# Optimization experiments

Hardware: AMD Instinct MI355X
Metric: run time of the kernel (lower is better)

Reference implementation:

```python
import jax, jax.numpy as jnp
import numpy as np

REG = 0.1          # entropic regularization, as in the module
N_ITERS = 100      # fixed Sinkhorn iteration count (POT numItermax capped; see notes)


def _sqdist(x, y):
    # ot.dist default: squared Euclidean pairwise distances, [n, m]
    x2 = jnp.sum(x * x, axis=1)[:, None]
    y2 = jnp.sum(y * y, axis=1)[None, :]
    M = x2 + y2 - 2.0 * (x @ y.T)
    return jnp.maximum(M, 0.0)


def setup_inputs() -> dict:
    key = jax.random.key(0)
    kx, ky = jax.random.split(key)
    n, m, d = 4096, 4096, 32
    # uniform in [0, 0.5) keeps exp(-M/reg) representable in fp32
    x = jax.random.uniform(kx, (n, d), dtype=jnp.float32) * 0.5
    y = jax.random.uniform(ky, (m, d), dtype=jnp.float32) * 0.5
    return {"x": x, "y": y}


def reference(x, y):
    n, m = x.shape[0], y.shape[0]
    a = jnp.full((n,), 1.0 / n, dtype=x.dtype)   # uniform source marginal
    b = jnp.full((m,), 1.0 / m, dtype=y.dtype)   # uniform target marginal
    M = _sqdist(x, y)                            # [n, m] cost
    K = jnp.exp(-M / REG)                        # [n, m] Gibbs kernel

    u0 = jnp.full((n,), 1.0 / n, dtype=x.dtype)
    v0 = jnp.full((m,), 1.0 / m, dtype=y.dtype)

    def step(carry, _):
        u, v = carry
        u = a / (K @ v)      # [n]
        v = b / (K.T @ u)    # [m]
        return (u, v), None

    (u, v), _ = jax.lax.scan(step, (u0, v0), None, length=N_ITERS)
    # transport plan gamma = diag(u) K diag(v), as returned by ot.bregman.sinkhorn
    gamma = u[:, None] * K * v[None, :]
    return gamma
```

## Files before the change

kernel.cpp:

```cpp
#include <hip/hip_runtime.h>
#include <hip/hip_fp16.h>


#define NN 4096
#define MM 4096
#define DD 32
#define N_ITERS 100

static constexpr float INV_REG = 10.0f;
static constexpr float A_MARG  = 1.0f / 4096.0f;
static constexpr float B_MARG  = 1.0f / 4096.0f;

typedef _Float16 h2_t __attribute__((ext_vector_type(2)));
typedef unsigned u32v4 __attribute__((ext_vector_type(4)));

static __device__ __forceinline__ float dot2(unsigned a, unsigned b, float acc) {
#if __has_builtin(__builtin_amdgcn_fdot2)
    return __builtin_amdgcn_fdot2(__builtin_bit_cast(h2_t, a),
                                  __builtin_bit_cast(h2_t, b), acc, false);
#else
    float2 fa = __half22float2(*(const __half2*)&a);
    float2 fb = __half22float2(*(const __half2*)&b);
    acc = fmaf(fa.x, fb.x, acc);
    return fmaf(fa.y, fb.y, acc);
#endif
}

static __device__ __forceinline__ uint4 ld_nt_u4(const uint4* p) {
#if __has_builtin(__builtin_nontemporal_load)
    u32v4 r = __builtin_nontemporal_load((const u32v4*)p);
    uint4 o; o.x = r[0]; o.y = r[1]; o.z = r[2]; o.w = r[3];
    return o;
#else
    return *p;
#endif
}

static __device__ __forceinline__ unsigned ld_dev_u32(const unsigned* p) {
    return __hip_atomic_load(p, __ATOMIC_RELAXED, __HIP_MEMORY_SCOPE_AGENT);
}
static __device__ __forceinline__ void st_dev_u32(unsigned* p, unsigned v) {
    __hip_atomic_store(p, v, __ATOMIC_RELAXED, __HIP_MEMORY_SCOPE_AGENT);
}
static __device__ __forceinline__ unsigned short ld_dev_u16(const unsigned short* p) {
    return __hip_atomic_load(p, __ATOMIC_RELAXED, __HIP_MEMORY_SCOPE_AGENT);
}
static __device__ __forceinline__ void st_dev_u16(unsigned short* p, unsigned short v) {
    __hip_atomic_store(p, v, __ATOMIC_RELAXED, __HIP_MEMORY_SCOPE_AGENT);
}
static __device__ __forceinline__ unsigned long long ld_dev_u64(const unsigned long long* p) {
    return __hip_atomic_load(p, __ATOMIC_RELAXED, __HIP_MEMORY_SCOPE_AGENT);
}

static __device__ __forceinline__ void gbar(unsigned* cnt8, unsigned p) {
    __syncthreads();
    if (threadIdx.x < 64) {
        const int l = threadIdx.x;
        if (l == 0) {
            asm volatile("s_waitcnt vmcnt(0)" ::: "memory");
            __hip_atomic_fetch_add(cnt8 + (blockIdx.x & 7) * 32, 1u,
                                   __ATOMIC_RELAXED, __HIP_MEMORY_SCOPE_AGENT);
        }
        const unsigned tgt = p * 64u;
        for (;;) {
            bool ok = true;
            if (l < 8)
                ok = (__hip_atomic_load(cnt8 + l * 32, __ATOMIC_RELAXED,
                                        __HIP_MEMORY_SCOPE_AGENT) >= tgt);
            if (__all(ok)) break;
            __builtin_amdgcn_s_sleep(1);
        }
    }
    __syncthreads();
}

__global__ void compute_K_half(const float* __restrict__ p, const float* __restrict__ q,
                               __half* __restrict__ Kh, __half* __restrict__ v16,
                               unsigned* __restrict__ conv, unsigned* __restrict__ slot,
                               unsigned* __restrict__ cnt8, int prime) {
    const int tid = threadIdx.x;
    const int j   = blockIdx.x * 256 + tid;
    const int r0  = blockIdx.y * 16;

    if (prime && blockIdx.y == 0) {
        v16[j] = __float2half(B_MARG);
        if (blockIdx.x == 0) {
            if (tid == 0) { *conv = 0u; *slot = 1u; }
            if (tid < 256) cnt8[tid] = 0u;
        }
    }

    float qv[DD];
    const float4* q4 = (const float4*)(q + (size_t)j * DD);
#pragma unroll
    for (int k = 0; k < DD / 4; ++k) {
        float4 t = q4[k];
        qv[4 * k + 0] = t.x; qv[4 * k + 1] = t.y;
        qv[4 * k + 2] = t.z; qv[4 * k + 3] = t.w;
    }

    __shared__ float ps[16 * DD];
    ps[tid]       = p[(size_t)r0 * DD + tid];
    ps[tid + 256] = p[(size_t)r0 * DD + tid + 256];
    __syncthreads();

#pragma unroll 4
    for (int ii = 0; ii < 16; ++ii) {
        float acc = 0.0f;
#pragma unroll
        for (int k = 0; k < DD; ++k) {
            float d = ps[ii * DD + k] - qv[k];
            acc = fmaf(d, d, acc);
        }
        Kh[(size_t)(r0 + ii) * MM + j] = __float2half(__expf(-acc * INV_REG));
    }
}

__global__ void __launch_bounds__(1024, 8)
sinkhorn_persist(const __half* __restrict__ Kh, const __half* __restrict__ KTh,
                 float* __restrict__ u32, __half* __restrict__ u16,
                 float* __restrict__ v32, __half* __restrict__ v16,
                 unsigned short* __restrict__ hist,
                 unsigned* __restrict__ slot, unsigned* __restrict__ cnt8) {
    __shared__ __align__(16) __half vlds[MM];
    __shared__ float part[16];
    const int tid  = threadIdx.x;
    const int lane = tid & 63;
    const int w    = tid >> 6;
    const int rib  = w >> 1;
    const int hlf  = w & 1;
    const int i    = blockIdx.x * 8 + rib;
    const int g0   = hlf * 256 + lane;
    const uint4* __restrict__ MU = (const uint4*)(Kh  + (size_t)i * MM);
    const uint4* __restrict__ MV = (const uint4*)(KTh + (size_t)i * MM);

    unsigned p = 0;

    uint4 k0 = MU[g0], k1 = MU[g0 + 64], k2 = MU[g0 + 128], k3 = MU[g0 + 192];

    for (int t = 0; t < N_ITERS; ++t) {
        if ((t & 1) == 0) {
            if (t != 0 && ld_dev_u32(slot) == 0u) break;
        } else {
            if (blockIdx.x == 0 && tid == 0) st_dev_u32(slot, 0u);
        }

        if (tid < 512) {
            const unsigned long long* s64 = (const unsigned long long*)v16;
            unsigned long long lo = ld_dev_u64(s64 + 2 * tid);
            unsigned long long hi = ld_dev_u64(s64 + 2 * tid + 1);
            ((unsigned long long*)vlds)[2 * tid]     = lo;
            ((unsigned long long*)vlds)[2 * tid + 1] = hi;
        }
        __syncthreads();
        {
            const uint4* V = (const uint4*)vlds;
            const uint4 a = V[g0], b = V[g0 + 64], c = V[g0 + 128], d = V[g0 + 192];
            float x0 = 0.f, x1 = 0.f, x2 = 0.f, x3 = 0.f;
            x0 = dot2(k0.x, a.x, x0); x0 = dot2(k0.y, a.y, x0);
            x0 = dot2(k0.z, a.z, x0); x0 = dot2(k0.w, a.w, x0);
            x1 = dot2(k1.x, b.x, x1); x1 = dot2(k1.y, b.y, x1);
            x1 = dot2(k1.z, b.z, x1); x1 = dot2(k1.w, b.w, x1);
            x2 = dot2(k2.x, c.x, x2); x2 = dot2(k2.y, c.y, x2);
            x2 = dot2(k2.z, c.z, x2); x2 = dot2(k2.w, c.w, x2);
            x3 = dot2(k3.x, d.x, x3); x3 = dot2(k3.y, d.y, x3);
            x3 = dot2(k3.z, d.z, x3); x3 = dot2(k3.w, d.w, x3);
            float acc = (x0 + x1) + (x2 + x3);
#pragma unroll
            for (int off = 32; off > 0; off >>= 1) acc += __shfl_down(acc, off, 64);
            if (lane == 0) part[w] = acc;
        }
        k0 = ld_nt_u4(MV + g0);
        k1 = ld_nt_u4(MV + g0 + 64);
        k2 = ld_nt_u4(MV + g0 + 128);
        k3 = ld_nt_u4(MV + g0 + 192);
        __syncthreads();
        if (tid < 8) {
            const int row = blockIdx.x * 8 + tid;
            float r = A_MARG / (part[2 * tid] + part[2 * tid + 1]);
            u32[row] = r;
            st_dev_u16((unsigned short*)u16 + row, __half_as_ushort(__float2half(r)));
        }
        gbar(cnt8, ++p);

        if (tid < 512) {
            const unsigned long long* s64 = (const unsigned long long*)u16;
            unsigned long long lo = ld_dev_u64(s64 + 2 * tid);
            unsigned long long hi = ld_dev_u64(s64 + 2 * tid + 1);
            ((unsigned long long*)vlds)[2 * tid]     = lo;
            ((unsigned long long*)vlds)[2 * tid + 1] = hi;
        }
        __syncthreads();
        {
            const uint4* V = (const uint4*)vlds;
            const uint4 a = V[g0], b = V[g0 + 64], c = V[g0 + 128], d = V[g0 + 192];
            float x0 = 0.f, x1 = 0.f, x2 = 0.f, x3 = 0.f;
            x0 = dot2(k0.x, a.x, x0); x0 = dot2(k0.y, a.y, x0);
            x0 = dot2(k0.z, a.z, x0); x0 = dot2(k0.w, a.w, x0);
            x1 = dot2(k1.x, b.x, x1); x1 = dot2(k1.y, b.y, x1);
            x1 = dot2(k1.z, b.z, x1); x1 = dot2(k1.w, b.w, x1);
            x2 = dot2(k2.x, c.x, x2); x2 = dot2(k2.y, c.y, x2);
            x2 = dot2(k2.z, c.z, x2); x2 = dot2(k2.w, c.w, x2);
            x3 = dot2(k3.x, d.x, x3); x3 = dot2(k3.y, d.y, x3);
            x3 = dot2(k3.z, d.z, x3); x3 = dot2(k3.w, d.w, x3);
            float acc = (x0 + x1) + (x2 + x3);
#pragma unroll
            for (int off = 32; off > 0; off >>= 1) acc += __shfl_down(acc, off, 64);
            if (lane == 0) part[w] = acc;
        }
        k0 = MU[g0]; k1 = MU[g0 + 64]; k2 = MU[g0 + 128]; k3 = MU[g0 + 192];
        __syncthreads();
        if (tid < 8) {
            const int row = blockIdx.x * 8 + tid;
            float r = B_MARG / (part[2 * tid] + part[2 * tid + 1]);
            v32[row] = r;
            const __half h = __float2half(r);
            const unsigned short bits = __half_as_ushort(h);
            if (t & 1) {
                const unsigned short old2 = ld_dev_u16(hist + row);
                if (old2 != bits) st_dev_u32(slot, 1u);
                st_dev_u16(hist + row, bits);
            }
            st_dev_u16((unsigned short*)v16 + row, bits);
        }
        gbar(cnt8, ++p);
    }
}

__global__ void __launch_bounds__(1024, 8)
rowpass_u(const __half* __restrict__ Mat, const __half* __restrict__ w16_in,
          float* __restrict__ w32_out, __half* __restrict__ w16_out,
          unsigned* __restrict__ conv, unsigned* __restrict__ slot, int t) {
    if (ld_dev_u32(conv)) return;
    if ((t & 1) == 0) {
        if (ld_dev_u32(slot) == 0u) {
            if (threadIdx.x == 0) st_dev_u32(conv, 1u);
            return;
        }
    } else {
        if (blockIdx.x == 0 && threadIdx.x == 0) st_dev_u32(slot, 0u);
    }

    __shared__ __align__(16) __half vlds[MM];
    __shared__ float part[16];
    const int tid  = threadIdx.x;
    const int lane = tid & 63;
    const int w    = tid >> 6;
    const int rib  = w >> 1;
    const int hlf  = w & 1;
    const int i    = blockIdx.x * 8 + rib;
    const uint4* __restrict__ Mrow = (const uint4*)(Mat + (size_t)i * MM);
    const int g0 = hlf * 256 + lane;

    uint4 stg;
    if (tid < 512) stg = ((const uint4*)w16_in)[tid];
    const uint4 k0 = Mrow[g0];
    const uint4 k1 = Mrow[g0 + 64];
    const uint4 k2 = Mrow[g0 + 128];
    const uint4 k3 = Mrow[g0 + 192];
    if (tid < 512) ((uint4*)vlds)[tid] = stg;
    __syncthreads();

    const uint4* V = (const uint4*)vlds;
    const uint4 v0 = V[g0];
    const uint4 v1 = V[g0 + 64];
    const uint4 v2 = V[g0 + 128];
    const uint4 v3 = V[g0 + 192];

    float a0 = 0.f, a1 = 0.f, a2 = 0.f, a3 = 0.f;
    a0 = dot2(k0.x, v0.x, a0); a0 = dot2(k0.y, v0.y, a0);
    a0 = dot2(k0.z, v0.z, a0); a0 = dot2(k0.w, v0.w, a0);
    a1 = dot2(k1.x, v1.x, a1); a1 = dot2(k1.y, v1.y, a1);
    a1 = dot2(k1.z, v1.z, a1); a1 = dot2(k1.w, v1.w, a1);
    a2 = dot2(k2.x, v2.x, a2); a2 = dot2(k2.y, v2.y, a2);
    a2 = dot2(k2.z, v2.z, a2); a2 = dot2(k2.w, v2.w, a2);
    a3 = dot2(k3.x, v3.x, a3); a3 = dot2(k3.y, v3.y, a3);
    a3 = dot2(k3.z, v3.z, a3); a3 = dot2(k3.w, v3.w, a3);
    float acc = (a0 + a1) + (a2 + a3);

#pragma unroll
    for (int off = 32; off > 0; off >>= 1) acc += __shfl_down(acc, off, 64);
    if (lane == 0) part[w] = acc;
    __syncthreads();

    if (tid < 8) {
        const int row = blockIdx.x * 8 + tid;
        float r = A_MARG / (part[2 * tid] + part[2 * tid + 1]);
        w32_out[row] = r;
        w16_out[row] = __float2half(r);
    }
}

__global__ void __launch_bounds__(1024, 8)
rowpass_v(const __half* __restrict__ Mat, const __half* __restrict__ w16_in,
          float* __restrict__ w32_out, __half* __restrict__ w16_out,
          unsigned short* __restrict__ hist,
          unsigned* __restrict__ conv, unsigned* __restrict__ slot, int t) {
    if (ld_dev_u32(conv)) return;

    __shared__ __align__(16) __half vlds[MM];
    __shared__ float part[16];
    const int tid  = threadIdx.x;
    const int lane = tid & 63;
    const int w    = tid >> 6;
    const int rib  = w >> 1;
    const int hlf  = w & 1;
    const int i    = blockIdx.x * 8 + rib;
    const uint4* __restrict__ Mrow = (const uint4*)(Mat + (size_t)i * MM);
    const int g0 = hlf * 256 + lane;

    uint4 stg;
    if (tid < 512) stg = ((const uint4*)w16_in)[tid];
    const uint4 k0 = Mrow[g0];
    const uint4 k1 = Mrow[g0 + 64];
    const uint4 k2 = Mrow[g0 + 128];
    const uint4 k3 = Mrow[g0 + 192];
    if (tid < 512) ((uint4*)vlds)[tid] = stg;
    __syncthreads();

    const uint4* V = (const uint4*)vlds;
    const uint4 v0 = V[g0];
    const uint4 v1 = V[g0 + 64];
    const uint4 v2 = V[g0 + 128];
    const uint4 v3 = V[g0 + 192];

    float a0 = 0.f, a1 = 0.f, a2 = 0.f, a3 = 0.f;
    a0 = dot2(k0.x, v0.x, a0); a0 = dot2(k0.y, v0.y, a0);
    a0 = dot2(k0.z, v0.z, a0); a0 = dot2(k0.w, v0.w, a0);
    a1 = dot2(k1.x, v1.x, a1); a1 = dot2(k1.y, v1.y, a1);
    a1 = dot2(k1.z, v1.z, a1); a1 = dot2(k1.w, v1.w, a1);
    a2 = dot2(k2.x, v2.x, a2); a2 = dot2(k2.y, v2.y, a2);
    a2 = dot2(k2.z, v2.z, a2); a2 = dot2(k2.w, v2.w, a2);
    a3 = dot2(k3.x, v3.x, a3); a3 = dot2(k3.y, v3.y, a3);
    a3 = dot2(k3.z, v3.z, a3); a3 = dot2(k3.w, v3.w, a3);
    float acc = (a0 + a1) + (a2 + a3);

#pragma unroll
    for (int off = 32; off > 0; off >>= 1) acc += __shfl_down(acc, off, 64);
    if (lane == 0) part[w] = acc;
    __syncthreads();

    if (tid < 8) {
        const int row = blockIdx.x * 8 + tid;
        float r = B_MARG / (part[2 * tid] + part[2 * tid + 1]);
        w32_out[row] = r;
        const __half h = __float2half(r);
        if (t & 1) {
            const unsigned short bits = __half_as_ushort(h);
            const unsigned short old2 = ld_dev_u16(hist + row);
            if (old2 != bits) st_dev_u32(slot, 1u);
            st_dev_u16(hist + row, bits);
        }
        w16_out[row] = h;
    }
}

__global__ void epilogue(const float* __restrict__ x, const float* __restrict__ y,
                         const float* __restrict__ u, const float* __restrict__ v,
                         float* __restrict__ out) {
    const int tid = threadIdx.x;
    const int j   = blockIdx.x * 256 + tid;
    const int r0  = blockIdx.y * 16;

    float yv[DD];
    const float4* y4 = (const float4*)(y + (size_t)j * DD);
#pragma unroll
    for (int k = 0; k < DD / 4; ++k) {
        float4 t = y4[k];
        yv[4 * k + 0] = t.x; yv[4 * k + 1] = t.y;
        yv[4 * k + 2] = t.z; yv[4 * k + 3] = t.w;
    }

    __shared__ float xs[16 * DD];
    __shared__ float u_lds[16];
    xs[tid]       = x[(size_t)r0 * DD + tid];
    xs[tid + 256] = x[(size_t)r0 * DD + tid + 256];
    if (tid < 16) u_lds[tid] = u[r0 + tid];
    __syncthreads();

    const float vj = v[j];
#pragma unroll 4
    for (int ii = 0; ii < 16; ++ii) {
        float acc = 0.0f;
#pragma unroll
        for (int k = 0; k < DD; ++k) {
            float d = xs[ii * DD + k] - yv[k];
            acc = fmaf(d, d, acc);
        }
        out[(size_t)(r0 + ii) * MM + j] = u_lds[ii] * __expf(-acc * INV_REG) * vj;
    }
}

extern "C" void kernel_launch(void* const* d_in, const int* in_sizes, int n_in,
                              void* d_out, int out_size, void* d_ws, size_t ws_size,
                              hipStream_t stream) {
    const float* x = (const float*)d_in[0];
    const float* y = (const float*)d_in[1];
    __half*   Kh   = (__half*)d_ws;
    __half*   KTh  = Kh + (size_t)NN * MM;
    float*    u32  = (float*)(KTh + (size_t)NN * MM);
    float*    v32  = u32 + NN;
    __half*   u16  = (__half*)(v32 + MM);
    __half*   v16  = u16 + NN;
    unsigned short* hist = (unsigned short*)(v16 + MM);
    unsigned* slot = (unsigned*)(hist + MM);
    unsigned* conv = slot + 1;
    unsigned* cnt8 = slot + 32;
    float*    out  = (float*)d_out;

    compute_K_half<<<dim3(MM / 256, NN / 16), 256, 0, stream>>>(x, y, Kh, v16, conv, slot, cnt8, 1);
    compute_K_half<<<dim3(NN / 256, MM / 16), 256, 0, stream>>>(y, x, KTh, v16, conv, slot, cnt8, 0);

    {
        void* args[] = { &Kh, &KTh, &u32, &u16, &v32, &v16, &hist, &slot, &cnt8 };
        hipError_t e = hipLaunchCooperativeKernel((const void*)sinkhorn_persist,
                                                  dim3(512), dim3(1024), args, 0, stream);
        if (e != hipSuccess) {
            (void)hipGetLastError();
            for (int t = 0; t < N_ITERS; ++t) {
                rowpass_u<<<NN / 8, 1024, 0, stream>>>(Kh,  v16, u32, u16, conv, slot, t);
                rowpass_v<<<MM / 8, 1024, 0, stream>>>(KTh, u16, v32, v16, hist, conv, slot, t);
            }
        }
    }

    epilogue<<<dim3(MM / 256, NN / 16), 256, 0, stream>>>(x, y, u32, v32, out);
}
```

Before: 637.5 us.

## Replace grid barrier with per-block tagged flags and packed data slots

Drops the centralized atomic-counter grid barrier. Each block now publishes its 8 half-precision results as two 64-bit words plus an iteration tag, and consumers spin on the per-producer tags before loading the data. Convergence detection is folded into a high bit of the tag, which removes the shared slot flag. Wave 0 delays its next matrix prefetch until after publishing, to shorten the critical path. The cost is 512 spinning threads per block and extra flag traffic, plus a reliance on relaxed-ordering memory semantics holding.

After: 621.4 us. 1.03x faster.

```diff
diff --git a/kernel.cpp b/kernel.cpp
--- a/kernel.cpp
+++ b/kernel.cpp
@@ -51,33 +51,15 @@
 static __device__ __forceinline__ unsigned long long ld_dev_u64(const unsigned long long* p) {
     return __hip_atomic_load(p, __ATOMIC_RELAXED, __HIP_MEMORY_SCOPE_AGENT);
 }
-
-static __device__ __forceinline__ void gbar(unsigned* cnt8, unsigned p) {
-    __syncthreads();
-    if (threadIdx.x < 64) {
-        const int l = threadIdx.x;
-        if (l == 0) {
-            asm volatile("s_waitcnt vmcnt(0)" ::: "memory");
-            __hip_atomic_fetch_add(cnt8 + (blockIdx.x & 7) * 32, 1u,
-                                   __ATOMIC_RELAXED, __HIP_MEMORY_SCOPE_AGENT);
-        }
-        const unsigned tgt = p * 64u;
-        for (;;) {
-            bool ok = true;
-            if (l < 8)
-                ok = (__hip_atomic_load(cnt8 + l * 32, __ATOMIC_RELAXED,
-                                        __HIP_MEMORY_SCOPE_AGENT) >= tgt);
-            if (__all(ok)) break;
-            __builtin_amdgcn_s_sleep(1);
-        }
-    }
-    __syncthreads();
+static __device__ __forceinline__ void st_dev_u64(unsigned long long* p, unsigned long long v) {
+    __hip_atomic_store(p, v, __ATOMIC_RELAXED, __HIP_MEMORY_SCOPE_AGENT);
 }
 
 __global__ void compute_K_half(const float* __restrict__ p, const float* __restrict__ q,
                                __half* __restrict__ Kh, __half* __restrict__ v16,
                                unsigned* __restrict__ conv, unsigned* __restrict__ slot,
-                               unsigned* __restrict__ cnt8, int prime) {
+                               unsigned* __restrict__ mtu, unsigned* __restrict__ mtv,
+                               int prime) {
     const int tid = threadIdx.x;
     const int j   = blockIdx.x * 256 + tid;
     const int r0  = blockIdx.y * 16;
@@ -86,7 +68,8 @@
         v16[j] = __float2half(B_MARG);
         if (blockIdx.x == 0) {
             if (tid == 0) { *conv = 0u; *slot = 1u; }
-            if (tid < 256) cnt8[tid] = 0u;
+            mtu[tid] = 0u; mtu[tid + 256] = 0u;
+            mtv[tid] = 0u; mtv[tid + 256] = 0u;
         }
     }
 
@@ -118,41 +101,62 @@
 
 __global__ void __launch_bounds__(1024, 8)
 sinkhorn_persist(const __half* __restrict__ Kh, const __half* __restrict__ KTh,
-                 float* __restrict__ u32, __half* __restrict__ u16,
-                 float* __restrict__ v32, __half* __restrict__ v16,
+                 float* __restrict__ u32g, float* __restrict__ v32g,
                  unsigned short* __restrict__ hist,
-                 unsigned* __restrict__ slot, unsigned* __restrict__ cnt8) {
+                 unsigned* __restrict__ mtu, unsigned* __restrict__ mtv,
+                 unsigned long long* __restrict__ mdu,
+                 unsigned long long* __restrict__ mdv) {
     __shared__ __align__(16) __half vlds[MM];
     __shared__ float part[16];
+    __shared__ unsigned fb_lds[8];
     const int tid  = threadIdx.x;
     const int lane = tid & 63;
     const int w    = tid >> 6;
     const int rib  = w >> 1;
     const int hlf  = w & 1;
-    const int i    = blockIdx.x * 8 + rib;
+    const int bid  = blockIdx.x;
+    const int i    = bid * 8 + rib;
     const int g0   = hlf * 256 + lane;
     const uint4* __restrict__ MU = (const uint4*)(Kh  + (size_t)i * MM);
     const uint4* __restrict__ MV = (const uint4*)(KTh + (size_t)i * MM);
 
-    unsigned p = 0;
-
     uint4 k0 = MU[g0], k1 = MU[g0 + 64], k2 = MU[g0 + 128], k3 = MU[g0 + 192];
 
     for (int t = 0; t < N_ITERS; ++t) {
-        if ((t & 1) == 0) {
-            if (t != 0 && ld_dev_u32(slot) == 0u) break;
+        if (t == 0) {
+            if (tid < 512) {
+                const unsigned long long dv =
+                    (unsigned long long)__half_as_ushort(__float2half(B_MARG)) *
+                    0x0001000100010001ULL;
+                ((unsigned long long*)vlds)[2 * tid]     = dv;
+                ((unsigned long long*)vlds)[2 * tid + 1] = dv;
+            }
+            __syncthreads();
         } else {
-            if (blockIdx.x == 0 && tid == 0) st_dev_u32(slot, 0u);
-        }
-
-        if (tid < 512) {
-            const unsigned long long* s64 = (const unsigned long long*)v16;
-            unsigned long long lo = ld_dev_u64(s64 + 2 * tid);
-            unsigned long long hi = ld_dev_u64(s64 + 2 * tid + 1);
-            ((unsigned long long*)vlds)[2 * tid]     = lo;
-            ((unsigned long long*)vlds)[2 * tid + 1] = hi;
-        }
-        __syncthreads();
+            if (tid < 512) {
+                const unsigned want = 2u * (unsigned)t;
+                unsigned tg;
+                for (;;) {
+                    tg = ld_dev_u32(mtv + tid);
+                    if ((tg & 0x7fffffffu) == want) break;
+                    __builtin_amdgcn_s_sleep(1);
+                }
+                asm volatile("" ::: "memory");
+                unsigned long long d0 = ld_dev_u64(mdv + 2 * tid);
+                unsigned long long d1 = ld_dev_u64(mdv + 2 * tid + 1);
+                ((unsigned long long*)vlds)[2 * tid]     = d0;
+                ((unsigned long long*)vlds)[2 * tid + 1] = d1;
+                const bool allf = __all((tg >> 31) != 0u);
+                if ((tid & 63) == 0) fb_lds[tid >> 6] = allf ? 1u : 0u;
+            }
+            __syncthreads();
+            if ((t & 1) == 0) {
+                if ((fb_lds[0] & fb_lds[1] & fb_lds[2] & fb_lds[3] &
+                     fb_lds[4] & fb_lds[5] & fb_lds[6] & fb_lds[7]) != 0u)
+                    break;
+            }
+        }
+
         {
             const uint4* V = (const uint4*)vlds;
             const uint4 a = V[g0], b = V[g0 + 64], c = V[g0 + 128], d = V[g0 + 192];
@@ -170,27 +174,47 @@
             for (int off = 32; off > 0; off >>= 1) acc += __shfl_down(acc, off, 64);
             if (lane == 0) part[w] = acc;
         }
-        k0 = ld_nt_u4(MV + g0);
-        k1 = ld_nt_u4(MV + g0 + 64);
-        k2 = ld_nt_u4(MV + g0 + 128);
-        k3 = ld_nt_u4(MV + g0 + 192);
+        if (w != 0) {
+            k0 = ld_nt_u4(MV + g0);       k1 = ld_nt_u4(MV + g0 + 64);
+            k2 = ld_nt_u4(MV + g0 + 128); k3 = ld_nt_u4(MV + g0 + 192);
+        }
         __syncthreads();
-        if (tid < 8) {
-            const int row = blockIdx.x * 8 + tid;
-            float r = A_MARG / (part[2 * tid] + part[2 * tid + 1]);
-            u32[row] = r;
-            st_dev_u16((unsigned short*)u16 + row, __half_as_ushort(__float2half(r)));
-        }
-        gbar(cnt8, ++p);
+        if (tid == 0) {
+            unsigned long long d0 = 0, d1 = 0;
+#pragma unroll
+            for (int q = 0; q < 8; ++q) {
+                float r = A_MARG / (part[2 * q] + part[2 * q + 1]);
+                u32g[bid * 8 + q] = r;
+                const unsigned long long h =
+                    (unsigned long long)__half_as_ushort(__float2half(r));
+                if (q < 4) d0 |= h << (16 * q); else d1 |= h << (16 * (q - 4));
+            }
+            st_dev_u64(mdu + 2 * bid,     d0);
+            st_dev_u64(mdu + 2 * bid + 1, d1);
+            asm volatile("s_waitcnt vmcnt(0)" ::: "memory");
+            st_dev_u32(mtu + bid, 2u * (unsigned)t + 1u);
+        }
+        if (w == 0) {
+            k0 = ld_nt_u4(MV + g0);       k1 = ld_nt_u4(MV + g0 + 64);
+            k2 = ld_nt_u4(MV + g0 + 128); k3 = ld_nt_u4(MV + g0 + 192);
+        }
 
         if (tid < 512) {
-            const unsigned long long* s64 = (const unsigned long long*)u16;
-            unsigned long long lo = ld_dev_u64(s64 + 2 * tid);
-            unsigned long long hi = ld_dev_u64(s64 + 2 * tid + 1);
-            ((unsigned long long*)vlds)[2 * tid]     = lo;
-            ((unsigned long long*)vlds)[2 * tid + 1] = hi;
+            const unsigned want = 2u * (unsigned)t + 1u;
+            unsigned tg;
+            for (;;) {
+                tg = ld_dev_u32(mtu + tid);
+                if ((tg & 0x7fffffffu) == want) break;
+                __builtin_amdgcn_s_sleep(1);
+            }
+            asm volatile("" ::: "memory");
+            unsigned long long d0 = ld_dev_u64(mdu + 2 * tid);
+            unsigned long long d1 = ld_dev_u64(mdu + 2 * tid + 1);
+            ((unsigned long long*)vlds)[2 * tid]     = d0;
+            ((unsigned long long*)vlds)[2 * tid + 1] = d1;
         }
         __syncthreads();
+
         {
             const uint4* V = (const uint4*)vlds;
             const uint4 a = V[g0], b = V[g0 + 64], c = V[g0 + 128], d = V[g0 + 192];
@@ -208,22 +232,36 @@
             for (int off = 32; off > 0; off >>= 1) acc += __shfl_down(acc, off, 64);
             if (lane == 0) part[w] = acc;
         }
-        k0 = MU[g0]; k1 = MU[g0 + 64]; k2 = MU[g0 + 128]; k3 = MU[g0 + 192];
+        if (w != 0) {
+            k0 = MU[g0]; k1 = MU[g0 + 64]; k2 = MU[g0 + 128]; k3 = MU[g0 + 192];
+        }
         __syncthreads();
-        if (tid < 8) {
-            const int row = blockIdx.x * 8 + tid;
-            float r = B_MARG / (part[2 * tid] + part[2 * tid + 1]);
-            v32[row] = r;
-            const __half h = __float2half(r);
-            const unsigned short bits = __half_as_ushort(h);
+        if (tid == 0) {
+            unsigned long long d0 = 0, d1 = 0;
+#pragma unroll
+            for (int q = 0; q < 8; ++q) {
+                float r = B_MARG / (part[2 * q] + part[2 * q + 1]);
+                v32g[bid * 8 + q] = r;
+                const unsigned long long h =
+                    (unsigned long long)__half_as_ushort(__float2half(r));
+                if (q < 4) d0 |= h << (16 * q); else d1 |= h << (16 * (q - 4));
+            }
+            unsigned tg = 2u * (unsigned)t + 2u;
             if (t & 1) {
-                const unsigned short old2 = ld_dev_u16(hist + row);
-                if (old2 != bits) st_dev_u32(slot, 1u);
-                st_dev_u16(hist + row, bits);
-            }
-            st_dev_u16((unsigned short*)v16 + row, bits);
-        }
-        gbar(cnt8, ++p);
+                unsigned long long h0 = ld_dev_u64((unsigned long long*)hist + 2 * bid);
+                unsigned long long h1 = ld_dev_u64((unsigned long long*)hist + 2 * bid + 1);
+                if (h0 == d0 && h1 == d1) tg |= 0x80000000u;
+                st_dev_u64((unsigned long long*)hist + 2 * bid,     d0);
+                st_dev_u64((unsigned long long*)hist + 2 * bid + 1, d1);
+            }
+            st_dev_u64(mdv + 2 * bid,     d0);
+            st_dev_u64(mdv + 2 * bid + 1, d1);
+            asm volatile("s_waitcnt vmcnt(0)" ::: "memory");
+            st_dev_u32(mtv + bid, tg);
+        }
+        if (w == 0) {
+            k0 = MU[g0]; k1 = MU[g0 + 64]; k2 = MU[g0 + 128]; k3 = MU[g0 + 192];
+        }
     }
 }
 
@@ -405,14 +443,17 @@
     unsigned short* hist = (unsigned short*)(v16 + MM);
     unsigned* slot = (unsigned*)(hist + MM);
     unsigned* conv = slot + 1;
-    unsigned* cnt8 = slot + 32;
+    unsigned* mtu  = slot + 512;
+    unsigned* mtv  = mtu + 512;
+    unsigned long long* mdu = (unsigned long long*)(mtv + 512);
+    unsigned long long* mdv = mdu + 1024;
     float*    out  = (float*)d_out;
 
-    compute_K_half<<<dim3(MM / 256, NN / 16), 256, 0, stream>>>(x, y, Kh, v16, conv, slot, cnt8, 1);
-    compute_K_half<<<dim3(NN / 256, MM / 16), 256, 0, stream>>>(y, x, KTh, v16, conv, slot, cnt8, 0);
+    compute_K_half<<<dim3(MM / 256, NN / 16), 256, 0, stream>>>(x, y, Kh, v16, conv, slot, mtu, mtv, 1);
+    compute_K_half<<<dim3(NN / 256, MM / 16), 256, 0, stream>>>(y, x, KTh, v16, conv, slot, mtu, mtv, 0);
 
     {
-        void* args[] = { &Kh, &KTh, &u32, &u16, &v32, &v16, &hist, &slot, &cnt8 };
+        void* args[] = { &Kh, &KTh, &u32, &v32, &hist, &mtu, &mtv, &mdu, &mdv };
         hipError_t e = hipLaunchCooperativeKernel((const void*)sinkhorn_persist,
                                                   dim3(512), dim3(1024), args, 0, stream);
         if (e != hipSuccess) {
```
